# Performance work log

Measured on AMD Instinct MI355X. Metric: run time of the kernel, lower is better.

The kernel has to match this reference:

```python
import jax, jax.numpy as jnp
import numpy as np

N = 50000
E = 800000
IN_C = 1024
HID = 64
HEADS = 4
OUT_C = 64
NEG_SLOPE = 0.2  # PyG GATConv default


def setup_inputs() -> dict:
    key = jax.random.key(0)
    ks = jax.random.split(key, 12)
    x = jax.random.normal(ks[0], (N, IN_C), dtype=jnp.float32)
    edge_index = jax.random.randint(ks[1], (2, E), 0, N, dtype=jnp.int64)
    s1 = 1.0 / np.sqrt(IN_C)
    s2 = 1.0 / np.sqrt(HEADS * HID)
    return {
        "x": x,
        "edge_index": edge_index,
        "W1": jax.random.normal(ks[2], (HEADS * HID, IN_C), dtype=jnp.float32) * s1,
        "a_src1": jax.random.normal(ks[3], (HEADS, HID), dtype=jnp.float32) * s2,
        "a_dst1": jax.random.normal(ks[4], (HEADS, HID), dtype=jnp.float32) * s2,
        "b1": jnp.zeros((HEADS * HID,), dtype=jnp.float32),
        "W2": jax.random.normal(ks[5], (OUT_C, HEADS * HID), dtype=jnp.float32) * s2,
        "a_src2": jax.random.normal(ks[6], (1, OUT_C), dtype=jnp.float32) * 0.1,
        "a_dst2": jax.random.normal(ks[7], (1, OUT_C), dtype=jnp.float32) * 0.1,
        "b2": jnp.zeros((OUT_C,), dtype=jnp.float32),
    }


def gat_conv(x, src, dst, W, a_src, a_dst, b, heads, concat):
    # x: [N, F_in]; src/dst: [E'] (self-loops already appended)
    n = x.shape[0]
    h = (x @ W.T).reshape(n, heads, -1)                 # [N, H, C]
    alpha_s = (h * a_src).sum(-1)                       # [N, H]
    alpha_d = (h * a_dst).sum(-1)                       # [N, H]
    e = jax.nn.leaky_relu(alpha_s[src] + alpha_d[dst], NEG_SLOPE)  # [E', H]
    # segment softmax over edges grouped by destination
    m = jax.ops.segment_max(e, dst, num_segments=n)     # [N, H]
    ex = jnp.exp(e - m[dst])
    denom = jax.ops.segment_sum(ex, dst, num_segments=n)
    alpha = ex / denom[dst]                             # [E', H]
    out = jax.ops.segment_sum(alpha[:, :, None] * h[src], dst, num_segments=n)  # [N, H, C]
    out = out.reshape(n, -1) if concat else out.mean(axis=1)
    return out + b


def reference(x, edge_index, W1, a_src1, a_dst1, b1, W2, a_src2, a_dst2, b2):
    n = x.shape[0]
    loop = jnp.arange(n, dtype=edge_index.dtype)
    src = jnp.concatenate([edge_index[0], loop])  # PyG add_self_loops=True
    dst = jnp.concatenate([edge_index[1], loop])
    # eval mode: dropout is identity
    h = gat_conv(x, src, dst, W1, a_src1, a_dst1, b1, HEADS, concat=True)
    h = jax.nn.elu(h)
    out = gat_conv(h, src, dst, W2, a_src2, a_dst2, b2, 1, concat=False)
    return out
```

## Files before the change

### kernel.cpp

```cpp
#include <hip/hip_runtime.h>
#include <hip/hip_bf16.h>
#include <math.h>

constexpr int IN_C = 1024;
constexpr int HEADS = 4;
constexpr int F1 = 256;
constexpr int OUT_C = 64;
constexpr float NEG = 0.2f;

using bf16x8 = __attribute__((ext_vector_type(8))) short;
using f32x4 = __attribute__((ext_vector_type(4))) float;

__device__ __forceinline__ float leaky(float x) { return x > 0.f ? x : NEG * x; }

__device__ __forceinline__ unsigned short bf16bits(float v) {
  __hip_bfloat16 b = __float2bfloat16(v);
  return *reinterpret_cast<unsigned short*>(&b);
}
__device__ __forceinline__ float bf2f(unsigned short u) {
  union { unsigned u; float f; } c; c.u = (unsigned)u << 16; return c.f;
}

#define GLD_LDS16(g, l)                                                        \
  __builtin_amdgcn_global_load_lds(                                            \
      (const __attribute__((address_space(1))) void*)(g),                      \
      (__attribute__((address_space(3))) void*)(l), 16, 0, 0)

constexpr int NB_W1 = (F1 * IN_C) / 256;
constexpr int NB_W2 = (OUT_C * F1) / 256;

__global__ __launch_bounds__(256) void prep_kernel(const float* __restrict__ W1,
                                                   unsigned short* __restrict__ W1b,
                                                   const float* __restrict__ W2,
                                                   unsigned short* __restrict__ W2b,
                                                   const int* __restrict__ ei, int E, int N,
                                                   int* __restrict__ deg) {
  int b = blockIdx.x;
  if (b < NB_W1) {
    int i = b * 256 + threadIdx.x;
    W1b[i] = bf16bits(W1[i]);
  } else if (b < NB_W1 + NB_W2) {
    int i = (b - NB_W1) * 256 + threadIdx.x;
    W2b[i] = bf16bits(W2[i]);
  } else {
    int e = (b - NB_W1 - NB_W2) * 256 + threadIdx.x;
    if (e < E + N) {
      int dst = (e < E) ? ei[E + e] : (e - E);
      atomicAdd(&deg[dst], 1);
    }
  }
}

__global__ __launch_bounds__(256, 3) void gemm1_mfma(const float* __restrict__ X,
                                                     const unsigned short* __restrict__ Wb,
                                                     unsigned short* __restrict__ Hb,
                                                     const float* __restrict__ a_src,
                                                     const float* __restrict__ a_dst,
                                                     float* __restrict__ as_out,
                                                     float* __restrict__ ad_out, int M, int MB2,
                                                     const int* __restrict__ ei, int E, int N,
                                                     const int* __restrict__ row_ptr,
                                                     int* __restrict__ fill,
                                                     int* __restrict__ col) {
  __shared__ float As4[128 * 64];
  __shared__ unsigned short Bs[128 * 64];
  const int tid = threadIdx.x;

  if (blockIdx.x >= MB2) {
    int e = (blockIdx.x - MB2) * 256 + tid;
    int ET = E + N;
    if (e < ET) {
      int src, dst;
      if (e < E) { src = ei[e]; dst = ei[E + e]; }
      else       { src = e - E; dst = e - E; }
      int pos = row_ptr[dst] + atomicAdd(&fill[dst], 1);
      col[pos] = src;
    }
    return;
  }

  const int rc = blockIdx.x >> 1;
  const int colg = blockIdx.x & 1;
  const int wave = tid >> 6;
  const int rg = wave >> 1;
  const int cg = wave & 1;
  const int lane = tid & 63;
  const int m15 = lane & 15;
  const int q = lane >> 4;
  const int bm = rc * 128;

  f32x4 acc[4][4];
#pragma unroll
  for (int i = 0; i < 4; ++i)
#pragma unroll
    for (int j = 0; j < 4; ++j) acc[i][j] = (f32x4){0.f, 0.f, 0.f, 0.f};

  for (int kt = 0; kt < IN_C; kt += 64) {
#pragma unroll
    for (int p = 0; p < 8; ++p) {
      int s = p * 256 + tid;
      int r = s >> 4;
      int cb = s & 15;
      int gr = (bm + r < M) ? (bm + r) : (M - 1);
      const float* g = X + (size_t)gr * IN_C + kt + ((cb ^ (r & 15)) << 2);
      GLD_LDS16(g, &As4[s * 4]);
    }
#pragma unroll
    for (int p = 0; p < 4; ++p) {
      int t = p * 256 + tid;
      int rB = t >> 3;
      int cbB = t & 7;
      const unsigned short* g = Wb + (size_t)(colg * 128 + rB) * IN_C + kt + ((cbB ^ (rB & 7)) << 3);
      GLD_LDS16(g, &Bs[t * 8]);
    }
    __syncthreads();

#pragma unroll
    for (int k0 = 0; k0 < 64; k0 += 32) {
      bf16x8 af[4], bfr[4];
#pragma unroll
      for (int i = 0; i < 4; ++i) {
        int ra = rg * 64 + i * 16 + m15;
        int c0 = (k0 >> 2) + q * 2;
        float4 f0 = *(const float4*)&As4[ra * 64 + ((c0 ^ (ra & 15)) << 2)];
        float4 f1 = *(const float4*)&As4[ra * 64 + (((c0 + 1) ^ (ra & 15)) << 2)];
        union { bf16x8 v; __hip_bfloat162 h[4]; } pk;
        pk.h[0] = __float22bfloat162_rn(make_float2(f0.x, f0.y));
        pk.h[1] = __float22bfloat162_rn(make_float2(f0.z, f0.w));
        pk.h[2] = __float22bfloat162_rn(make_float2(f1.x, f1.y));
        pk.h[3] = __float22bfloat162_rn(make_float2(f1.z, f1.w));
        af[i] = pk.v;
      }
#pragma unroll
      for (int j = 0; j < 4; ++j) {
        int rb = cg * 64 + j * 16 + m15;
        int cbp = ((k0 >> 3) + q) ^ (rb & 7);
        bfr[j] = *(const bf16x8*)&Bs[rb * 64 + cbp * 8];
      }
#pragma unroll
      for (int i = 0; i < 4; ++i)
#pragma unroll
        for (int j = 0; j < 4; ++j)
          acc[i][j] = __builtin_amdgcn_mfma_f32_16x16x32_bf16(af[i], bfr[j], acc[i][j], 0, 0, 0);
    }
    __syncthreads();
  }

  const int cbase = colg * 128 + cg * 64;
  const int head = colg * 2 + cg;
  float asf[4], adf[4];
#pragma unroll
  for (int j = 0; j < 4; ++j) {
    asf[j] = a_src[cbase + j * 16 + m15];
    adf[j] = a_dst[cbase + j * 16 + m15];
  }
#pragma unroll
  for (int i = 0; i < 4; ++i) {
#pragma unroll
    for (int r = 0; r < 4; ++r) {
      int row = bm + rg * 64 + i * 16 + q * 4 + r;
      if (row < M) {
#pragma unroll
        for (int j = 0; j < 4; ++j)
          Hb[(size_t)row * F1 + cbase + j * 16 + m15] = bf16bits(acc[i][j][r]);
      }
      float s = acc[i][0][r] * asf[0] + acc[i][1][r] * asf[1] +
                acc[i][2][r] * asf[2] + acc[i][3][r] * asf[3];
      float d = acc[i][0][r] * adf[0] + acc[i][1][r] * adf[1] +
                acc[i][2][r] * adf[2] + acc[i][3][r] * adf[3];
#pragma unroll
      for (int o = 1; o < 16; o <<= 1) {
        s += __shfl_xor(s, o, 64);
        d += __shfl_xor(d, o, 64);
      }
      if (m15 == 0 && row < M) {
        as_out[row * HEADS + head] = s;
        ad_out[row * HEADS + head] = d;
      }
    }
  }
}

__global__ __launch_bounds__(256, 4) void gemm2_mfma(const unsigned short* __restrict__ Y,
                                                     const unsigned short* __restrict__ W2b,
                                                     float* __restrict__ H2,
                                                     const float* __restrict__ a_src,
                                                     const float* __restrict__ a_dst,
                                                     float* __restrict__ as_out,
                                                     float* __restrict__ ad_out, int M) {
  __shared__ unsigned short As[64 * 64];
  __shared__ unsigned short Bs[64 * 64];
  const int tid = threadIdx.x;
  const int wave = tid >> 6;
  const int lane = tid & 63;
  const int m15 = lane & 15;
  const int q = lane >> 4;
  const int bm = blockIdx.x * 64;

  f32x4 acc[4];
#pragma unroll
  for (int j = 0; j < 4; ++j) acc[j] = (f32x4){0.f, 0.f, 0.f, 0.f};

  for (int kt = 0; kt < F1; kt += 64) {
#pragma unroll
    for (int p = 0; p < 2; ++p) {
      int s = p * 256 + tid;
      int r = s >> 3;
      int cb = s & 7;
      int colo = (cb ^ (r & 7)) << 3;
      int gr = (bm + r < M) ? (bm + r) : (M - 1);
      GLD_LDS16(Y + (size_t)gr * F1 + kt + colo, &As[(p * 256 + wave * 64) * 8]);
      GLD_LDS16(W2b + (size_t)r * F1 + kt + colo, &Bs[(p * 256 + wave * 64) * 8]);
    }
    __syncthreads();
#pragma unroll
    for (int k0 = 0; k0 < 64; k0 += 32) {
      int ra = wave * 16 + m15;
      bf16x8 af = *(const bf16x8*)&As[ra * 64 + ((((k0 >> 3) + q) ^ (ra & 7)) << 3)];
      bf16x8 bfr[4];
#pragma unroll
      for (int j = 0; j < 4; ++j) {
        int rb = j * 16 + m15;
        bfr[j] = *(const bf16x8*)&Bs[rb * 64 + ((((k0 >> 3) + q) ^ (rb & 7)) << 3)];
      }
#pragma unroll
      for (int j = 0; j < 4; ++j)
        acc[j] = __builtin_amdgcn_mfma_f32_16x16x32_bf16(af, bfr[j], acc[j], 0, 0, 0);
    }
    __syncthreads();
  }
  float asf[4], adf[4];
#pragma unroll
  for (int j = 0; j < 4; ++j) {
    asf[j] = a_src[j * 16 + m15];
    adf[j] = a_dst[j * 16 + m15];
  }
#pragma unroll
  for (int r = 0; r < 4; ++r) {
    int row = bm + wave * 16 + q * 4 + r;
    if (row < M) {
#pragma unroll
      for (int j = 0; j < 4; ++j) H2[(size_t)row * OUT_C + j * 16 + m15] = acc[j][r];
    }
    float s = acc[0][r] * asf[0] + acc[1][r] * asf[1] + acc[2][r] * asf[2] + acc[3][r] * asf[3];
    float d = acc[0][r] * adf[0] + acc[1][r] * adf[1] + acc[2][r] * adf[2] + acc[3][r] * adf[3];
#pragma unroll
    for (int o = 1; o < 16; o <<= 1) {
      s += __shfl_xor(s, o, 64);
      d += __shfl_xor(d, o, 64);
    }
    if (m15 == 0 && row < M) {
      as_out[row] = s;
      ad_out[row] = d;
    }
  }
}

__global__ __launch_bounds__(256) void scan_block_sums(const int* __restrict__ deg,
                                                       int* __restrict__ part, int n) {
  __shared__ int sm[256];
  int t = threadIdx.x;
  int i = blockIdx.x * 256 + t;
  sm[t] = (i < n) ? deg[i] : 0;
  __syncthreads();
  for (int off = 128; off > 0; off >>= 1) {
    if (t < off) sm[t] += sm[t + off];
    __syncthreads();
  }
  if (t == 0) part[blockIdx.x] = sm[0];
}

__global__ __launch_bounds__(256) void scan_final2(const int* __restrict__ deg,
                                                   const int* __restrict__ part,
                                                   int* __restrict__ row_ptr, int n) {
  __shared__ int sm[256];
  __shared__ int wsum[4];
  int t = threadIdx.x;
  int i = blockIdx.x * 256 + t;
  sm[t] = (i < n) ? deg[i] : 0;
  int pv = (t < blockIdx.x) ? part[t] : 0;
#pragma unroll
  for (int o = 1; o < 64; o <<= 1) pv += __shfl_xor(pv, o, 64);
  if ((t & 63) == 0) wsum[t >> 6] = pv;
  __syncthreads();
  for (int off = 1; off < 256; off <<= 1) {
    int u = (t >= off) ? sm[t - off] : 0;
    __syncthreads();
    sm[t] += u;
    __syncthreads();
  }
  int base = wsum[0] + wsum[1] + wsum[2] + wsum[3];
  if (i < n) row_ptr[i + 1] = base + sm[t];
  if (i == 0) row_ptr[0] = 0;
}

__global__ __launch_bounds__(256) void agg1_kernel(const unsigned short* __restrict__ hb,
                                                   const float* __restrict__ as,
                                                   const float* __restrict__ ad,
                                                   const int* __restrict__ row_ptr,
                                                   const int* __restrict__ col,
                                                   const float* __restrict__ bias,
                                                   unsigned short* __restrict__ yb, int N) {
  int dst = (blockIdx.x * blockDim.x + threadIdx.x) >> 6;
  int lane = threadIdx.x & 63;
  if (dst >= N) return;
  const int s0 = row_ptr[dst], s1 = row_ptr[dst + 1];
  const int par = lane >> 5;
  const int cg = lane & 31;
  const int hh = cg >> 3;
  const float adl = ad[dst * 4 + hh];
  float acc[8];
#pragma unroll
  for (int k = 0; k < 8; ++k) acc[k] = 0.f;
  float den = 0.f;

  int i = s0 + par;
  for (; i + 6 < s1; i += 8) {
    int sA = col[i], sB = col[i + 2], sC = col[i + 4], sD = col[i + 6];
    float wA = __expf(leaky(as[sA * 4 + hh] + adl));
    float wB = __expf(leaky(as[sB * 4 + hh] + adl));
    float wC = __expf(leaky(as[sC * 4 + hh] + adl));
    float wD = __expf(leaky(as[sD * 4 + hh] + adl));
    uint4 hA = *(const uint4*)(hb + (size_t)sA * F1 + cg * 8);
    uint4 hB = *(const uint4*)(hb + (size_t)sB * F1 + cg * 8);
    uint4 hC = *(const uint4*)(hb + (size_t)sC * F1 + cg * 8);
    uint4 hD = *(const uint4*)(hb + (size_t)sD * F1 + cg * 8);
    den += (wA + wB) + (wC + wD);
    const unsigned short* pa = (const unsigned short*)&hA;
    const unsigned short* pb = (const unsigned short*)&hB;
    const unsigned short* pc = (const unsigned short*)&hC;
    const unsigned short* pd = (const unsigned short*)&hD;
#pragma unroll
    for (int k = 0; k < 8; ++k) {
      acc[k] = fmaf(wA, bf2f(pa[k]), acc[k]);
      acc[k] = fmaf(wB, bf2f(pb[k]), acc[k]);
      acc[k] = fmaf(wC, bf2f(pc[k]), acc[k]);
      acc[k] = fmaf(wD, bf2f(pd[k]), acc[k]);
    }
  }
  for (; i + 2 < s1; i += 4) {
    int sA = col[i], sB = col[i + 2];
    float wA = __expf(leaky(as[sA * 4 + hh] + adl));
    float wB = __expf(leaky(as[sB * 4 + hh] + adl));
    uint4 hA = *(const uint4*)(hb + (size_t)sA * F1 + cg * 8);
    uint4 hB = *(const uint4*)(hb + (size_t)sB * F1 + cg * 8);
    den += wA + wB;
    const unsigned short* pa = (const unsigned short*)&hA;
    const unsigned short* pb = (const unsigned short*)&hB;
#pragma unroll
    for (int k = 0; k < 8; ++k) {
      acc[k] = fmaf(wA, bf2f(pa[k]), acc[k]);
      acc[k] = fmaf(wB, bf2f(pb[k]), acc[k]);
    }
  }
  for (; i < s1; i += 2) {
    int s = col[i];
    float w = __expf(leaky(as[s * 4 + hh] + adl));
    uint4 hv = *(const uint4*)(hb + (size_t)s * F1 + cg * 8);
    den += w;
    const unsigned short* p = (const unsigned short*)&hv;
#pragma unroll
    for (int k = 0; k < 8; ++k) acc[k] = fmaf(w, bf2f(p[k]), acc[k]);
  }
  den += __shfl_xor(den, 32, 64);
#pragma unroll
  for (int k = 0; k < 8; ++k) acc[k] += __shfl_xor(acc[k], 32, 64);

  if (par == 0) {
    const float iv = 1.f / den;
    float4 b0 = *(const float4*)(bias + cg * 8);
    float4 b1 = *(const float4*)(bias + cg * 8 + 4);
    float bv[8] = {b0.x, b0.y, b0.z, b0.w, b1.x, b1.y, b1.z, b1.w};
    ushort4 o[2];
    unsigned short* po = (unsigned short*)o;
#pragma unroll
    for (int k = 0; k < 8; ++k) {
      float v = acc[k] * iv + bv[k];
      v = v > 0.f ? v : (__expf(v) - 1.f);
      po[k] = bf16bits(v);
    }
    *(uint4*)(yb + (size_t)dst * F1 + cg * 8) = *(uint4*)o;
  }
}

__global__ __launch_bounds__(256) void agg2_kernel(const float* __restrict__ h,
                                                   const float* __restrict__ as,
                                                   const float* __restrict__ ad,
                                                   const int* __restrict__ row_ptr,
                                                   const int* __restrict__ col,
                                                   const float* __restrict__ bias,
                                                   float* __restrict__ out, int N) {
  int dst = (blockIdx.x * blockDim.x + threadIdx.x) >> 6;
  int lane = threadIdx.x & 63;
  if (dst >= N) return;
  const int s0 = row_ptr[dst], s1 = row_ptr[dst + 1];
  const int par = lane >> 5;
  const int cg = lane & 31;
  const float adl = ad[dst];
  float a0 = 0.f, a1 = 0.f, den = 0.f;

  int i = s0 + par;
  for (; i + 6 < s1; i += 8) {
    int sA = col[i], sB = col[i + 2], sC = col[i + 4], sD = col[i + 6];
    float wA = __expf(leaky(as[sA] + adl));
    float wB = __expf(leaky(as[sB] + adl));
    float wC = __expf(leaky(as[sC] + adl));
    float wD = __expf(leaky(as[sD] + adl));
    float2 hA = *(const float2*)(h + (size_t)sA * OUT_C + cg * 2);
    float2 hB = *(const float2*)(h + (size_t)sB * OUT_C + cg * 2);
    float2 hC = *(const float2*)(h + (size_t)sC * OUT_C + cg * 2);
    float2 hD = *(const float2*)(h + (size_t)sD * OUT_C + cg * 2);
    den += (wA + wB) + (wC + wD);
    a0 = fmaf(wA, hA.x, a0); a1 = fmaf(wA, hA.y, a1);
    a0 = fmaf(wB, hB.x, a0); a1 = fmaf(wB, hB.y, a1);
    a0 = fmaf(wC, hC.x, a0); a1 = fmaf(wC, hC.y, a1);
    a0 = fmaf(wD, hD.x, a0); a1 = fmaf(wD, hD.y, a1);
  }
  for (; i + 2 < s1; i += 4) {
    int sA = col[i], sB = col[i + 2];
    float wA = __expf(leaky(as[sA] + adl));
    float wB = __expf(leaky(as[sB] + adl));
    float2 hA = *(const float2*)(h + (size_t)sA * OUT_C + cg * 2);
    float2 hB = *(const float2*)(h + (size_t)sB * OUT_C + cg * 2);
    den += wA + wB;
    a0 = fmaf(wA, hA.x, a0); a1 = fmaf(wA, hA.y, a1);
    a0 = fmaf(wB, hB.x, a0); a1 = fmaf(wB, hB.y, a1);
  }
  for (; i < s1; i += 2) {
    int s = col[i];
    float w = __expf(leaky(as[s] + adl));
    float2 hv = *(const float2*)(h + (size_t)s * OUT_C + cg * 2);
    den += w;
    a0 = fmaf(w, hv.x, a0); a1 = fmaf(w, hv.y, a1);
  }
  den += __shfl_xor(den, 32, 64);
  a0 += __shfl_xor(a0, 32, 64);
  a1 += __shfl_xor(a1, 32, 64);
  if (par == 0) {
    const float iv = 1.f / den;
    float2 bv = *(const float2*)(bias + cg * 2);
    float2 o = make_float2(a0 * iv + bv.x, a1 * iv + bv.y);
    *(float2*)(out + (size_t)dst * OUT_C + cg * 2) = o;
  }
}

extern "C" void kernel_launch(void* const* d_in, const int* in_sizes, int n_in,
                              void* d_out, int out_size, void* d_ws, size_t ws_size,
                              hipStream_t stream) {
  const float* x      = (const float*)d_in[0];
  const int*   ei     = (const int*)d_in[1];
  const float* W1     = (const float*)d_in[2];
  const float* a_src1 = (const float*)d_in[3];
  const float* a_dst1 = (const float*)d_in[4];
  const float* b1     = (const float*)d_in[5];
  const float* W2     = (const float*)d_in[6];
  const float* a_src2 = (const float*)d_in[7];
  const float* a_dst2 = (const float*)d_in[8];
  const float* b2     = (const float*)d_in[9];
  float* out = (float*)d_out;

  const int N = in_sizes[0] / IN_C;
  const int E = in_sizes[1] / 2;
  const int ET = E + N;

  char* ws = (char*)d_ws;
  size_t off = 0;
  auto alloc = [&](size_t bytes) -> void* {
    void* p = ws + off;
    off = (off + bytes + 255) & ~(size_t)255;
    return p;
  };
  unsigned short* h1b = (unsigned short*)alloc((size_t)N * F1 * 2);
  unsigned short* y1b = (unsigned short*)alloc((size_t)N * F1 * 2);
  float* h2      = (float*)alloc((size_t)N * OUT_C * 4);
  float* as1     = (float*)alloc((size_t)N * HEADS * 4);
  float* ad1     = (float*)alloc((size_t)N * HEADS * 4);
  float* as2     = (float*)alloc((size_t)N * 4);
  float* ad2     = (float*)alloc((size_t)N * 4);
  int*   deg     = (int*)alloc((size_t)N * 2 * 4);
  int*   fill    = deg + N;
  int*   row_ptr = (int*)alloc((size_t)(N + 1) * 4);
  int*   col     = (int*)alloc((size_t)ET * 4);
  int*   part    = (int*)alloc(1024 * 4);
  unsigned short* W1b = (unsigned short*)alloc((size_t)F1 * IN_C * 2);
  unsigned short* W2b = (unsigned short*)alloc((size_t)OUT_C * F1 * 2);
  (void)off; (void)ws_size; (void)n_in; (void)out_size;

  hipMemsetAsync(deg, 0, (size_t)N * 2 * 4, stream);

  const int NBD = (ET + 255) / 256;
  const int P = (N + 255) / 256;

  prep_kernel<<<NB_W1 + NB_W2 + NBD, 256, 0, stream>>>(W1, W1b, W2, W2b, ei, E, N, deg);
  scan_block_sums<<<P, 256, 0, stream>>>(deg, part, N);
  scan_final2<<<P, 256, 0, stream>>>(deg, part, row_ptr, N);

  const int NB4 = (N + 3) / 4;
  const int MB2 = ((N + 127) / 128) * 2;
  const int SB = (ET + 255) / 256;

  gemm1_mfma<<<MB2 + SB, 256, 0, stream>>>(x, W1b, h1b, a_src1, a_dst1, as1, ad1, N, MB2,
                                           ei, E, N, row_ptr, fill, col);
  agg1_kernel<<<NB4, 256, 0, stream>>>(h1b, as1, ad1, row_ptr, col, b1, y1b, N);

  gemm2_mfma<<<(N + 63) / 64, 256, 0, stream>>>(y1b, W2b, h2, a_src2, a_dst2, as2, ad2, N);
  agg2_kernel<<<NB4, 256, 0, stream>>>(h2, as2, ad2, row_ptr, col, b2, out, N);
}
```

Baseline: 504.3 us.

## Double-buffer gemm1 tiles with register-staged bf16 A conversion and 512 threads

Restructures the first GEMM to 512-thread blocks with 8 waves each owning a 32x64 sub-tile. Shared memory is double-buffered so loads for the next K-slab overlap MFMA work on the current one. The fp32 X tile is now loaded into registers, converted to bf16 once, and written to LDS, instead of staging fp32 in LDS and converting on every fragment read. This halves A's LDS footprint and removes repeated conversion, at the cost of register pressure from the prefetched values and a changed occupancy target.

```diff
diff --git a/kernel.cpp b/kernel.cpp
--- a/kernel.cpp
+++ b/kernel.cpp
@@ -51,7 +51,7 @@
   }
 }
 
-__global__ __launch_bounds__(256, 3) void gemm1_mfma(const float* __restrict__ X,
+__global__ __launch_bounds__(512, 4) void gemm1_mfma(const float* __restrict__ X,
                                                      const unsigned short* __restrict__ Wb,
                                                      unsigned short* __restrict__ Hb,
                                                      const float* __restrict__ a_src,
@@ -62,12 +62,14 @@
                                                      const int* __restrict__ row_ptr,
                                                      int* __restrict__ fill,
                                                      int* __restrict__ col) {
-  __shared__ float As4[128 * 64];
-  __shared__ unsigned short Bs[128 * 64];
+  __shared__ unsigned short As0[128 * 64];
+  __shared__ unsigned short As1[128 * 64];
+  __shared__ unsigned short Bs0[128 * 64];
+  __shared__ unsigned short Bs1[128 * 64];
   const int tid = threadIdx.x;
 
   if (blockIdx.x >= MB2) {
-    int e = (blockIdx.x - MB2) * 256 + tid;
+    int e = (blockIdx.x - MB2) * 512 + tid;
     int ET = E + N;
     if (e < ET) {
       int src, dst;
@@ -89,62 +91,97 @@
   const int q = lane >> 4;
   const int bm = rc * 128;
 
-  f32x4 acc[4][4];
-#pragma unroll
-  for (int i = 0; i < 4; ++i)
+  const int sA0 = tid, sA1 = 512 + tid;
+  const int rA0 = sA0 >> 3, cA0 = sA0 & 7;
+  const int rA1 = sA1 >> 3, cA1 = sA1 & 7;
+  const int grA0 = (bm + rA0 < M) ? (bm + rA0) : (M - 1);
+  const int grA1 = (bm + rA1 < M) ? (bm + rA1) : (M - 1);
+  const float* aSrc0 = X + (size_t)grA0 * IN_C + ((cA0 ^ (rA0 & 7)) << 3);
+  const float* aSrc1 = X + (size_t)grA1 * IN_C + ((cA1 ^ (rA1 & 7)) << 3);
+  const int rB0 = sA0 >> 3, cB0 = sA0 & 7;
+  const int rB1 = sA1 >> 3, cB1 = sA1 & 7;
+  const unsigned short* bSrc0 = Wb + (size_t)(colg * 128 + rB0) * IN_C + ((cB0 ^ (rB0 & 7)) << 3);
+  const unsigned short* bSrc1 = Wb + (size_t)(colg * 128 + rB1) * IN_C + ((cB1 ^ (rB1 & 7)) << 3);
+
+  f32x4 acc[2][4];
+#pragma unroll
+  for (int i = 0; i < 2; ++i)
 #pragma unroll
     for (int j = 0; j < 4; ++j) acc[i][j] = (f32x4){0.f, 0.f, 0.f, 0.f};
 
-  for (int kt = 0; kt < IN_C; kt += 64) {
-#pragma unroll
-    for (int p = 0; p < 8; ++p) {
-      int s = p * 256 + tid;
-      int r = s >> 4;
-      int cb = s & 15;
-      int gr = (bm + r < M) ? (bm + r) : (M - 1);
-      const float* g = X + (size_t)gr * IN_C + kt + ((cb ^ (r & 15)) << 2);
-      GLD_LDS16(g, &As4[s * 4]);
-    }
-#pragma unroll
-    for (int p = 0; p < 4; ++p) {
-      int t = p * 256 + tid;
-      int rB = t >> 3;
-      int cbB = t & 7;
-      const unsigned short* g = Wb + (size_t)(colg * 128 + rB) * IN_C + kt + ((cbB ^ (rB & 7)) << 3);
-      GLD_LDS16(g, &Bs[t * 8]);
-    }
-    __syncthreads();
-
-#pragma unroll
-    for (int k0 = 0; k0 < 64; k0 += 32) {
-      bf16x8 af[4], bfr[4];
-#pragma unroll
-      for (int i = 0; i < 4; ++i) {
-        int ra = rg * 64 + i * 16 + m15;
-        int c0 = (k0 >> 2) + q * 2;
-        float4 f0 = *(const float4*)&As4[ra * 64 + ((c0 ^ (ra & 15)) << 2)];
-        float4 f1 = *(const float4*)&As4[ra * 64 + (((c0 + 1) ^ (ra & 15)) << 2)];
-        union { bf16x8 v; __hip_bfloat162 h[4]; } pk;
-        pk.h[0] = __float22bfloat162_rn(make_float2(f0.x, f0.y));
-        pk.h[1] = __float22bfloat162_rn(make_float2(f0.z, f0.w));
-        pk.h[2] = __float22bfloat162_rn(make_float2(f1.x, f1.y));
-        pk.h[3] = __float22bfloat162_rn(make_float2(f1.z, f1.w));
-        af[i] = pk.v;
-      }
-#pragma unroll
-      for (int j = 0; j < 4; ++j) {
-        int rb = cg * 64 + j * 16 + m15;
-        int cbp = ((k0 >> 3) + q) ^ (rb & 7);
-        bfr[j] = *(const bf16x8*)&Bs[rb * 64 + cbp * 8];
-      }
-#pragma unroll
-      for (int i = 0; i < 4; ++i)
-#pragma unroll
-        for (int j = 0; j < 4; ++j)
-          acc[i][j] = __builtin_amdgcn_mfma_f32_16x16x32_bf16(af[i], bfr[j], acc[i][j], 0, 0, 0);
-    }
-    __syncthreads();
-  }
+  float4 f00, f01, f10, f11;
+
+#define A_LOAD(KT)                                                             \
+  f00 = *(const float4*)(aSrc0 + (KT));                                        \
+  f01 = *(const float4*)(aSrc0 + (KT) + 4);                                    \
+  f10 = *(const float4*)(aSrc1 + (KT));                                        \
+  f11 = *(const float4*)(aSrc1 + (KT) + 4);
+
+#define B_STAGE(KT, BS)                                                        \
+  GLD_LDS16(bSrc0 + (KT), &BS[sA0 * 8]);                                       \
+  GLD_LDS16(bSrc1 + (KT), &BS[sA1 * 8]);
+
+#define A_WRITE(AS)                                                            \
+  {                                                                            \
+    union { uint4 u; __hip_bfloat162 h[4]; } pk;                               \
+    pk.h[0] = __float22bfloat162_rn(make_float2(f00.x, f00.y));                \
+    pk.h[1] = __float22bfloat162_rn(make_float2(f00.z, f00.w));                \
+    pk.h[2] = __float22bfloat162_rn(make_float2(f01.x, f01.y));                \
+    pk.h[3] = __float22bfloat162_rn(make_float2(f01.z, f01.w));                \
+    *(uint4*)&AS[sA0 * 8] = pk.u;                                              \
+    pk.h[0] = __float22bfloat162_rn(make_float2(f10.x, f10.y));                \
+    pk.h[1] = __float22bfloat162_rn(make_float2(f10.z, f10.w));                \
+    pk.h[2] = __float22bfloat162_rn(make_float2(f11.x, f11.y));                \
+    pk.h[3] = __float22bfloat162_rn(make_float2(f11.z, f11.w));                \
+    *(uint4*)&AS[sA1 * 8] = pk.u;                                              \
+  }
+
+#define COMPUTE(AS, BS)                                                        \
+  {                                                                            \
+    _Pragma("unroll")                                                          \
+    for (int k0 = 0; k0 < 64; k0 += 32) {                                      \
+      bf16x8 af[2], bfr[4];                                                    \
+      _Pragma("unroll")                                                        \
+      for (int i = 0; i < 2; ++i) {                                            \
+        int ra = rg * 32 + i * 16 + m15;                                       \
+        af[i] = *(const bf16x8*)&AS[ra * 64 + ((((k0 >> 3) + q) ^ (ra & 7)) << 3)]; \
+      }                                                                        \
+      _Pragma("unroll")                                                        \
+      for (int j = 0; j < 4; ++j) {                                            \
+        int rb = cg * 64 + j * 16 + m15;                                       \
+        bfr[j] = *(const bf16x8*)&BS[rb * 64 + ((((k0 >> 3) + q) ^ (rb & 7)) << 3)]; \
+      }                                                                        \
+      _Pragma("unroll")                                                        \
+      for (int i = 0; i < 2; ++i)                                              \
+        _Pragma("unroll")                                                      \
+        for (int j = 0; j < 4; ++j)                                            \
+          acc[i][j] = __builtin_amdgcn_mfma_f32_16x16x32_bf16(af[i], bfr[j], acc[i][j], 0, 0, 0); \
+    }                                                                          \
+  }
+
+  A_LOAD(0);
+  B_STAGE(0, Bs0);
+  A_WRITE(As0);
+  __syncthreads();
+
+  for (int kt = 0; kt < IN_C; kt += 128) {
+    A_LOAD(kt + 64);
+    B_STAGE(kt + 64, Bs1);
+    COMPUTE(As0, Bs0);
+    A_WRITE(As1);
+    __syncthreads();
+    if (kt + 128 < IN_C) {
+      A_LOAD(kt + 128);
+      B_STAGE(kt + 128, Bs0);
+    }
+    COMPUTE(As1, Bs1);
+    if (kt + 128 < IN_C) { A_WRITE(As0); }
+    __syncthreads();
+  }
+#undef A_LOAD
+#undef B_STAGE
+#undef A_WRITE
+#undef COMPUTE
 
   const int cbase = colg * 128 + cg * 64;
   const int head = colg * 2 + cg;
@@ -155,10 +192,10 @@
     adf[j] = a_dst[cbase + j * 16 + m15];
   }
 #pragma unroll
-  for (int i = 0; i < 4; ++i) {
+  for (int i = 0; i < 2; ++i) {
 #pragma unroll
     for (int r = 0; r < 4; ++r) {
-      int row = bm + rg * 64 + i * 16 + q * 4 + r;
+      int row = bm + rg * 32 + i * 16 + q * 4 + r;
       if (row < M) {
 #pragma unroll
         for (int j = 0; j < 4; ++j)
@@ -497,9 +534,9 @@
 
   const int NB4 = (N + 3) / 4;
   const int MB2 = ((N + 127) / 128) * 2;
-  const int SB = (ET + 255) / 256;
-
-  gemm1_mfma<<<MB2 + SB, 256, 0, stream>>>(x, W1b, h1b, a_src1, a_dst1, as1, ad1, N, MB2,
+  const int SB = (ET + 511) / 512;
+
+  gemm1_mfma<<<MB2 + SB, 512, 0, stream>>>(x, W1b, h1b, a_src1, a_dst1, as1, ad1, N, MB2,
                                            ei, E, N, row_ptr, fill, col);
   agg1_kernel<<<NB4, 256, 0, stream>>>(h1b, as1, ad1, row_ptr, col, b1, y1b, N);
 
```

After: 499.9 us. Within noise of the previous version (-0.9%).
